# Performance work log

Measured on AMD Instinct MI355X. Metric: run time of the kernel, lower is better.

## Reference

```python
import jax, jax.numpy as jnp
import numpy as np

LAMBD = 1.0
N_CLASSES = 1000


def setup_inputs() -> dict:
    key = jax.random.key(0)
    k1, k2, k3 = jax.random.split(key, 3)
    B, D, C = 32768, 128, N_CLASSES
    embeddings = jax.random.normal(k1, (B, D), dtype=jnp.float32)
    targets = jax.random.randint(k2, (B,), 0, C, dtype=jnp.int64)
    centers = jax.random.normal(k3, (C, D), dtype=jnp.float32)
    return {"embeddings": embeddings, "targets": targets, "centers": centers}


def reference(embeddings, targets, centers):
    # Original code round-trips embeddings through numpy -> data_mat is detached.
    e = jax.lax.stop_gradient(embeddings)  # [B, D]
    B = e.shape[0]
    C = centers.shape[0]
    # intra-class distance: exact per-sample gather + squared diff
    own_centers = centers[targets]                         # [B, D]
    dis_intra = jnp.sum((e - own_centers) ** 2, axis=1)    # [B]
    # all-pairs squared distances via expansion (avoids [B, C, D] intermediate)
    e_sq = jnp.sum(e * e, axis=1)                          # [B]
    c_sq = jnp.sum(centers * centers, axis=1)              # [C]
    cross = jnp.einsum('bd,cd->bc', e, centers)            # [B, C]
    dis_all = e_sq[:, None] + c_sq[None, :] - 2.0 * cross  # [B, C]
    # margin terms over non-target classes only
    mask = targets[:, None] != jnp.arange(C)[None, :]      # [B, C] True where j != y_i
    terms = jax.nn.relu(LAMBD + dis_intra[:, None] - dis_all)
    loss = jnp.sum(jnp.where(mask, terms, 0.0)) / (B * (C - 1))
    return loss
```

## Files before the change

kernel.cpp:

```cpp
#include <hip/hip_runtime.h>

#define DD 128
#define NTC 8
#define NCOPY 8
#define COPYBYTES (NTC * 16384)
#define BM 32

typedef __attribute__((ext_vector_type(4))) float f32x4;
typedef long long i64;

typedef __attribute__((address_space(1))) const void gvoid_t;
typedef __attribute__((address_space(3))) void svoid_t;
#define GLOAD_LDS16(g, s) __builtin_amdgcn_global_load_lds((gvoid_t*)(g), (svoid_t*)(s), 16, 0, 0)

__device__ __forceinline__ unsigned pk8(float a, float b, float c, float d) {
    int v = __builtin_amdgcn_cvt_pk_fp8_f32(a, b, 0, false);
    v = __builtin_amdgcn_cvt_pk_fp8_f32(c, d, v, true);
    return (unsigned)v;
}

__global__ void prep_centers(const float* __restrict__ ctr,
                             unsigned char* __restrict__ wsB,
                             float* __restrict__ csqh, int C, int Cpad) {
    int gid = blockIdx.x * 256 + threadIdx.x;
    int col = gid >> 4, q = (gid >> 2) & 3, cpg = gid & 3;
    if (col >= Cpad) return;
    const float* src = ctr + (size_t)col * DD + q * 32;
    const int r = col & 127;
    const unsigned tbase = (unsigned)(col >> 7) * 16384u + (unsigned)r * 128u;
    const unsigned sw = ((unsigned)r & 15u) << 3;
    float cs = 0.f;
    uint2 uu[4];
    #pragma unroll
    for (int m = 0; m < 4; ++m) {
        float4 v0 = make_float4(0.f,0.f,0.f,0.f), v1 = v0;
        if (col < C) {
            v0 = *(const float4*)(src + m * 8);
            v1 = *(const float4*)(src + m * 8 + 4);
        }
        cs = fmaf(v0.x,v0.x,cs); cs = fmaf(v0.y,v0.y,cs);
        cs = fmaf(v0.z,v0.z,cs); cs = fmaf(v0.w,v0.w,cs);
        cs = fmaf(v1.x,v1.x,cs); cs = fmaf(v1.y,v1.y,cs);
        cs = fmaf(v1.z,v1.z,cs); cs = fmaf(v1.w,v1.w,cs);
        uu[m].x = pk8(v0.x, v0.y, v0.z, v0.w);
        uu[m].y = pk8(v1.x, v1.y, v1.z, v1.w);
    }
    unsigned char* dst0 = wsB + (unsigned)(2*cpg)   * (unsigned)COPYBYTES + tbase;
    unsigned char* dst1 = wsB + (unsigned)(2*cpg+1) * (unsigned)COPYBYTES + tbase;
    #pragma unroll
    for (int m = 0; m < 4; ++m) {
        unsigned off = (((unsigned)(q * 4 + m)) * 8u) ^ sw;
        *(uint2*)(dst0 + off) = uu[m];
        *(uint2*)(dst1 + off) = uu[m];
    }
    cs += __shfl_xor(cs, 4); cs += __shfl_xor(cs, 8);
    if (q == 0) {
        float v = (col < C) ? 0.5f * cs : 1e30f;
        csqh[(2*cpg)   * 1024 + col] = v;
        csqh[(2*cpg+1) * 1024 + col] = v;
    }
}

__global__ __launch_bounds__(256, 4) void center_mfma(
    const float* __restrict__ emb, const int* __restrict__ tgt,
    const float* __restrict__ ctr, const unsigned char* __restrict__ wsB,
    const float* __restrict__ csqh, float* __restrict__ partials)
{
    __shared__ uint4 sB4[2048];
    __shared__ uint4 sA4[256];
    __shared__ float sRT[BM];
    __shared__ float sRed[4];
    unsigned char* sAb = (unsigned char*)sA4;
    unsigned char* sB0 = (unsigned char*)sB4;
    unsigned char* sB1 = sB0 + 16384;

    const int t = threadIdx.x;
    const int row0 = blockIdx.x * BM;
    const int cp = blockIdx.x & (NCOPY - 1);
    const unsigned char* wsBx = wsB + (size_t)cp * COPYBYTES;
    const float* csqx = csqh + cp * 1024;

    const int l  = t & 63;
    const int wc = t >> 6;
    const int li = l & 15;
    const int lh = l >> 4;
    const unsigned sw = (unsigned)li << 3;

    const int r = t >> 3, q8 = t & 7;
    const float* srcE = emb + (size_t)(row0 + r) * DD + q8 * 16;
    const int y = tgt[row0 + r];
    const float* srcC = ctr + (size_t)y * DD + q8 * 16;
    float4 ev[4], cv[4];
    #pragma unroll
    for (int m = 0; m < 4; ++m) ev[m] = *(const float4*)(srcE + m * 4);
    #pragma unroll
    for (int m = 0; m < 4; ++m) cv[m] = *(const float4*)(srcC + m * 4);
    float cqa[NTC], cqb[NTC];
    #pragma unroll
    for (int nt = 0; nt < NTC; ++nt) {
        cqa[nt] = csqx[nt*128 + wc*32 + li];
        cqb[nt] = csqx[nt*128 + wc*32 + 16 + li];
    }
    __builtin_amdgcn_sched_barrier(0);

    #pragma unroll
    for (int i = 0; i < 4; ++i) {
        unsigned off = (unsigned)(i * 256 + t) * 16u;
        GLOAD_LDS16(wsBx + off, sB0 + off);
    }
    __builtin_amdgcn_sched_barrier(0);

    {
        const unsigned swA = ((unsigned)r & 15u) << 3;
        float se = 0.f, sd = 0.f;
        #pragma unroll
        for (int m = 0; m < 4; ++m) {
            float4 e0 = ev[m], c0 = cv[m];
            se = fmaf(e0.x,e0.x,se); se = fmaf(e0.y,e0.y,se);
            se = fmaf(e0.z,e0.z,se); se = fmaf(e0.w,e0.w,se);
            float d;
            d = e0.x-c0.x; sd = fmaf(d,d,sd);  d = e0.y-c0.y; sd = fmaf(d,d,sd);
            d = e0.z-c0.z; sd = fmaf(d,d,sd);  d = e0.w-c0.w; sd = fmaf(d,d,sd);
        }
        #pragma unroll
        for (int m = 0; m < 2; ++m) {
            float4 e0 = ev[2*m], e1 = ev[2*m+1];
            uint2 u;
            u.x = pk8(e0.x, e0.y, e0.z, e0.w);
            u.y = pk8(e1.x, e1.y, e1.z, e1.w);
            unsigned j = (unsigned)(q8 * 2 + m);
            *(uint2*)(sAb + (unsigned)r * 128u + ((8u * j) ^ swA)) = u;
        }
        se += __shfl_xor(se, 1); se += __shfl_xor(se, 2); se += __shfl_xor(se, 4);
        sd += __shfl_xor(sd, 1); sd += __shfl_xor(sd, 2); sd += __shfl_xor(sd, 4);
        if (q8 == 0) sRT[r] = 0.5f * (1.0f + sd - se);
    }
    __syncthreads();

    i64 aF[2][4];
    #pragma unroll
    for (int mf = 0; mf < 2; ++mf)
        #pragma unroll
        for (int ks = 0; ks < 4; ++ks)
            aF[mf][ks] = *(const i64*)(sAb + (unsigned)(16*mf + li) * 128u +
                                       (((unsigned)(8*lh + 32*ks)) ^ sw));
    float rtv[8];
    #pragma unroll
    for (int mf = 0; mf < 2; ++mf)
        #pragma unroll
        for (int rr = 0; rr < 4; ++rr)
            rtv[mf*4+rr] = sRT[16*mf + 4*lh + rr];

    float tsum = 0.f;

    #pragma unroll
    for (int nt = 0; nt < NTC; ++nt) {
        unsigned char* bufR = (nt & 1) ? sB1 : sB0;
        unsigned char* bufW = (nt & 1) ? sB0 : sB1;

        __syncthreads();

        if (nt + 1 < NTC) {
            const unsigned char* g = wsBx + (size_t)(nt + 1) * 16384;
            #pragma unroll
            for (int i = 0; i < 4; ++i) {
                unsigned off = (unsigned)(i * 256 + t) * 16u;
                GLOAD_LDS16(g + off, bufW + off);
            }
        }

        i64 bF0[4], bF1[4];
        #pragma unroll
        for (int ks = 0; ks < 4; ++ks) {
            unsigned kof = ((unsigned)(8*lh + 32*ks)) ^ sw;
            bF0[ks] = *(const i64*)(bufR + (unsigned)(wc*32 + li) * 128u + kof);
            bF1[ks] = *(const i64*)(bufR + (unsigned)(wc*32 + 16 + li) * 128u + kof);
        }

        f32x4 acc[2][2];
        #pragma unroll
        for (int mf = 0; mf < 2; ++mf)
            #pragma unroll
            for (int rr = 0; rr < 4; ++rr) {
                acc[mf][0][rr] = rtv[mf*4+rr] - cqa[nt];
                acc[mf][1][rr] = rtv[mf*4+rr] - cqb[nt];
            }

        #pragma unroll
        for (int ks = 0; ks < 4; ++ks)
            #pragma unroll
            for (int mf = 0; mf < 2; ++mf) {
                acc[mf][0] = __builtin_amdgcn_mfma_f32_16x16x32_fp8_fp8(aF[mf][ks], bF0[ks], acc[mf][0], 0, 0, 0);
                acc[mf][1] = __builtin_amdgcn_mfma_f32_16x16x32_fp8_fp8(aF[mf][ks], bF1[ks], acc[mf][1], 0, 0, 0);
            }

        float s0 = 0.f, s1 = 0.f;
        #pragma unroll
        for (int mf = 0; mf < 2; ++mf)
            #pragma unroll
            for (int rr = 0; rr < 4; ++rr) {
                s0 = fmaf(2.0f, fmaxf(acc[mf][0][rr], 0.f), s0);
                s1 = fmaf(2.0f, fmaxf(acc[mf][1][rr], 0.f), s1);
            }
        tsum += s0 + s1;
    }

    float s = tsum;
    #pragma unroll
    for (int off = 32; off; off >>= 1) s += __shfl_down(s, off);
    if (l == 0) sRed[wc] = s;
    __syncthreads();
    if (t == 0) partials[blockIdx.x] = sRed[0] + sRed[1] + sRed[2] + sRed[3];
}

__global__ void reduce_k(const float* __restrict__ partials, int n,
                         float* __restrict__ out, double diagSub, double invDenom) {
    __shared__ double sRed[4];
    int t = threadIdx.x;
    double s = 0.0;
    for (int i = t; i < n; i += 256) s += (double)partials[i];
    #pragma unroll
    for (int off = 32; off; off >>= 1) s += __shfl_down(s, off);
    if ((t & 63) == 0) sRed[t >> 6] = s;
    __syncthreads();
    if (t == 0) out[0] = (float)(((sRed[0]+sRed[1]+sRed[2]+sRed[3]) - diagSub) * invDenom);
}

extern "C" void kernel_launch(void* const* d_in, const int* in_sizes, int n_in,
                              void* d_out, int out_size, void* d_ws, size_t ws_size,
                              hipStream_t stream) {
    const float* emb = (const float*)d_in[0];
    const int*   tgt = (const int*)d_in[1];
    const float* ctr = (const float*)d_in[2];

    const int B = in_sizes[1];
    const int C = in_sizes[2] / DD;
    const int Cpad = NTC * 128;
    const int nblk = B / BM;

    unsigned char* wsB = (unsigned char*)d_ws;
    float* csqh = (float*)(wsB + (size_t)NCOPY * COPYBYTES);
    float* partials = csqh + NCOPY * 1024;

    prep_centers<<<(Cpad * 16) / 256, 256, 0, stream>>>(ctr, wsB, csqh, C, Cpad);
    center_mfma<<<nblk, 256, 0, stream>>>(emb, tgt, ctr, wsB, csqh, partials);
    reduce_k<<<1, 256, 0, stream>>>(partials, nblk, (float*)d_out,
                                    (double)B,
                                    1.0 / ((double)B * (double)(C - 1)));
}
```

Measured before the change: 23.27 us.

## Load B fragments directly from global in fragment-major layout, drop LDS staging

The prep kernel now writes centers in a per-wave, per-lane fragment-ordered layout, so each lane fetches its two B fragments for a k-step with one 16-byte global load. The main kernel no longer double-buffers center tiles through LDS with global_load_lds and no longer needs per-tile __syncthreads. This removes the LDS traffic and barriers, and the lower LDS footprint may allow more blocks per CU. In exchange the kernel relies on L2/L1 hits for the repeated center reads, and global-load latency is exposed directly inside the MFMA loop with no explicit prefetch.

Result: slower. 46.07 us (+98.0%).

```diff
diff --git a/kernel.cpp b/kernel.cpp
--- a/kernel.cpp
+++ b/kernel.cpp
@@ -8,10 +8,7 @@
 
 typedef __attribute__((ext_vector_type(4))) float f32x4;
 typedef long long i64;
-
-typedef __attribute__((address_space(1))) const void gvoid_t;
-typedef __attribute__((address_space(3))) void svoid_t;
-#define GLOAD_LDS16(g, s) __builtin_amdgcn_global_load_lds((gvoid_t*)(g), (svoid_t*)(s), 16, 0, 0)
+typedef __attribute__((ext_vector_type(2))) long long i64x2;
 
 __device__ __forceinline__ unsigned pk8(float a, float b, float c, float d) {
     int v = __builtin_amdgcn_cvt_pk_fp8_f32(a, b, 0, false);
@@ -26,9 +23,11 @@
     int col = gid >> 4, q = (gid >> 2) & 3, cpg = gid & 3;
     if (col >= Cpad) return;
     const float* src = ctr + (size_t)col * DD + q * 32;
-    const int r = col & 127;
-    const unsigned tbase = (unsigned)(col >> 7) * 16384u + (unsigned)r * 128u;
-    const unsigned sw = ((unsigned)r & 15u) << 3;
+    const int colr = col & 127;
+    const int wcg = colr >> 5, rem = colr & 31;
+    const int half = rem >> 4, li_ = rem & 15;
+    const unsigned fbase = (unsigned)(col >> 7) * 16384u + (unsigned)wcg * 4096u +
+                           (unsigned)q * 1024u + (unsigned)li_ * 16u + (unsigned)half * 8u;
     float cs = 0.f;
     uint2 uu[4];
     #pragma unroll
@@ -45,13 +44,12 @@
         uu[m].x = pk8(v0.x, v0.y, v0.z, v0.w);
         uu[m].y = pk8(v1.x, v1.y, v1.z, v1.w);
     }
-    unsigned char* dst0 = wsB + (unsigned)(2*cpg)   * (unsigned)COPYBYTES + tbase;
-    unsigned char* dst1 = wsB + (unsigned)(2*cpg+1) * (unsigned)COPYBYTES + tbase;
+    unsigned char* dst0 = wsB + (unsigned)(2*cpg)   * (unsigned)COPYBYTES + fbase;
+    unsigned char* dst1 = wsB + (unsigned)(2*cpg+1) * (unsigned)COPYBYTES + fbase;
     #pragma unroll
     for (int m = 0; m < 4; ++m) {
-        unsigned off = (((unsigned)(q * 4 + m)) * 8u) ^ sw;
-        *(uint2*)(dst0 + off) = uu[m];
-        *(uint2*)(dst1 + off) = uu[m];
+        *(uint2*)(dst0 + (unsigned)m * 256u) = uu[m];
+        *(uint2*)(dst1 + (unsigned)m * 256u) = uu[m];
     }
     cs += __shfl_xor(cs, 4); cs += __shfl_xor(cs, 8);
     if (q == 0) {
@@ -66,13 +64,10 @@
     const float* __restrict__ ctr, const unsigned char* __restrict__ wsB,
     const float* __restrict__ csqh, float* __restrict__ partials)
 {
-    __shared__ uint4 sB4[2048];
     __shared__ uint4 sA4[256];
     __shared__ float sRT[BM];
     __shared__ float sRed[4];
     unsigned char* sAb = (unsigned char*)sA4;
-    unsigned char* sB0 = (unsigned char*)sB4;
-    unsigned char* sB1 = sB0 + 16384;
 
     const int t = threadIdx.x;
     const int row0 = blockIdx.x * BM;
@@ -101,14 +96,6 @@
         cqa[nt] = csqx[nt*128 + wc*32 + li];
         cqb[nt] = csqx[nt*128 + wc*32 + 16 + li];
     }
-    __builtin_amdgcn_sched_barrier(0);
-
-    #pragma unroll
-    for (int i = 0; i < 4; ++i) {
-        unsigned off = (unsigned)(i * 256 + t) * 16u;
-        GLOAD_LDS16(wsBx + off, sB0 + off);
-    }
-    __builtin_amdgcn_sched_barrier(0);
 
     {
         const unsigned swA = ((unsigned)r & 15u) << 3;
@@ -151,30 +138,18 @@
         for (int rr = 0; rr < 4; ++rr)
             rtv[mf*4+rr] = sRT[16*mf + 4*lh + rr];
 
+    const unsigned char* gB = wsBx + (unsigned)wc * 4096u + (unsigned)l * 16u;
+
     float tsum = 0.f;
 
     #pragma unroll
     for (int nt = 0; nt < NTC; ++nt) {
-        unsigned char* bufR = (nt & 1) ? sB1 : sB0;
-        unsigned char* bufW = (nt & 1) ? sB0 : sB1;
-
-        __syncthreads();
-
-        if (nt + 1 < NTC) {
-            const unsigned char* g = wsBx + (size_t)(nt + 1) * 16384;
-            #pragma unroll
-            for (int i = 0; i < 4; ++i) {
-                unsigned off = (unsigned)(i * 256 + t) * 16u;
-                GLOAD_LDS16(g + off, bufW + off);
-            }
-        }
-
         i64 bF0[4], bF1[4];
         #pragma unroll
         for (int ks = 0; ks < 4; ++ks) {
-            unsigned kof = ((unsigned)(8*lh + 32*ks)) ^ sw;
-            bF0[ks] = *(const i64*)(bufR + (unsigned)(wc*32 + li) * 128u + kof);
-            bF1[ks] = *(const i64*)(bufR + (unsigned)(wc*32 + 16 + li) * 128u + kof);
+            i64x2 v = *(const i64x2*)(gB + (unsigned)nt * 16384u + (unsigned)ks * 1024u);
+            bF0[ks] = v.x;
+            bF1[ks] = v.y;
         }
 
         f32x4 acc[2][2];
```
